# Performance work log

Measured on AMD Instinct MI355X. Metric: run time of the kernel, lower is better.

Reference implementation:

```python
import jax, jax.numpy as jnp
import numpy as np

H, QK, V, HID = 24, 16, 16, 128
EPS = 1e-6


def setup_inputs() -> dict:
    key = jax.random.key(0)
    ks = jax.random.split(key, 12)
    N, L = 2, 512
    s = 0.05
    inp = {
        "x": jax.random.normal(ks[0], (N, L, HID), jnp.float32),
        "R": jax.random.normal(ks[1], (N, L, 3, 3), jnp.float32),
        "t": jax.random.normal(ks[2], (N, L, 3), jnp.float32) * 10.0,
        "mask": jnp.ones((N, L), bool),
        # torch nn.Linear weights are (out_features, in_features)
        "Wq": jax.random.normal(ks[3], (H * QK, HID), jnp.float32) * s,
        "Wk": jax.random.normal(ks[4], (H * QK, HID), jnp.float32) * s,
        "Wv": jax.random.normal(ks[5], (H * V, HID), jnp.float32) * s,
        "bv": jnp.zeros((H * V,), jnp.float32),
        "Wa": jax.random.normal(ks[6], (3 * H, HID), jnp.float32) * s,
        "ba": jnp.full((3 * H,), EPS, jnp.float32),
        "Wb": jax.random.normal(ks[7], (3 * H, HID), jnp.float32) * s,
        "bb": jnp.full((3 * H,), EPS, jnp.float32),
        "Wp": jax.random.normal(ks[8], (HID, (V + 5) * H), jnp.float32) * s,
        "bp": jnp.zeros((HID,), jnp.float32),
        "alpha": -2.0 * jnp.ones((1, H, 1, 1), jnp.float32),
        "beta": -2.0 * jnp.ones((1, H, 1, 1), jnp.float32),
    }
    return inp


def reference(x, R, t, mask, Wq, Wk, Wv, bv, Wa, ba, Wb, bb, Wp, bp, alpha, beta):
    N, L, _ = x.shape
    al = jax.nn.softplus(alpha)  # (1,H,1,1)
    be = jax.nn.softplus(beta)

    a = (x @ Wa.T + ba).reshape(N, L, H, 1, 3).transpose(0, 2, 1, 3, 4)  # (N,H,L,1,3)
    b = (x @ Wb.T + bb).reshape(N, L, H, 1, 3).transpose(0, 2, 1, 3, 4)  # (N,H,L,1,3)

    # to_local: express t_j in local frame of residue i -> R_i^T (t_j - t_i)
    rel = t[:, None, :, :] - t[:, :, None, :]              # (N,L,L,3)
    local = jnp.einsum('nidx,nijd->nijx', R, rel)          # (N,L,L,3)

    r = local[:, None] - b                                  # (N,H,L,L,3)
    r_size = jnp.sqrt(jnp.sum(r * r, axis=-1))              # (N,H,L,L)
    a_size = jnp.sqrt(jnp.sum(a * a, axis=-1))              # (N,H,L,1)
    r_dot_a = jnp.sum(r * a, axis=-1)                       # (N,H,L,L)
    theta = jnp.arccos(r_dot_a / ((r_size + EPS) * (a_size + EPS)))

    ray_w = -al * r_size - be * theta                       # (N,H,L,L)

    q = (x @ Wq.T).reshape(N, L, H, QK)
    k = (x @ Wk.T).reshape(N, L, H, QK)
    std_w = jnp.einsum('nihd,njhd->nhij', q, k) * (QK ** -0.5)

    att = (2.0 ** -0.5) * (ray_w + std_w)
    diag = jnp.eye(L, dtype=bool)
    att = jnp.where(diag[None, None], jnp.asarray(-100.0, att.dtype), att)
    att = jnp.where(mask[:, None, None, :], att, -jnp.inf)
    att = jax.nn.softmax(att, axis=-1)                      # (N,H,L,L)

    v = (x @ Wv.T + bv).reshape(N, L, H, V)
    v_aggr = jnp.einsum('nhij,njhd->nihd', att, v)          # (N,L,H,V)
    r_aggr = jnp.einsum('nhij,nhijd->nihd', att, r)         # (N,L,H,3)
    r_aggr_size = jnp.sqrt(jnp.sum(r_aggr * r_aggr, axis=-1))  # (N,L,H)
    theta_aggr = jnp.einsum('nhij,nhij->nih', att, theta)   # (N,L,H)

    concat = jnp.concatenate([
        v_aggr.reshape(N, L, -1),
        r_aggr.reshape(N, L, -1),
        r_aggr_size,
        theta_aggr,
    ], axis=-1)                                             # (N,L,(V+5)*H)
    return concat @ Wp.T + bp
```

## Files before the change

kernel.cpp:

```cpp
#include <hip/hip_runtime.h>
#include <math.h>

#define NHEAD 24
#define LEN   512
#define NB    2
#define HID   128
#define EPSI  1e-6f

static constexpr size_t QKV_SZ = (size_t)NB * NHEAD * LEN * 16;
static constexpr size_t AB_SZ  = (size_t)NB * NHEAD * LEN * 3;
static constexpr size_t Q_OFF = 0;
static constexpr size_t K_OFF = QKV_SZ;
static constexpr size_t V_OFF = 2 * QKV_SZ;
static constexpr size_t A_OFF = 3 * QKV_SZ;
static constexpr size_t B_OFF = A_OFF + AB_SZ;
static constexpr size_t C_OFF = B_OFF + AB_SZ;

#define QSCALE2 0.25504597f
#define SCL     1.02020406f
#define CSHIFT  (-14.4269504f)

__device__ __forceinline__ float fast_exp2(float x) {
    return __builtin_amdgcn_exp2f(x);
}

__global__ __launch_bounds__(256) void proj_kernel(
    const float* __restrict__ x,
    const float* __restrict__ Wq, const float* __restrict__ Wk,
    const float* __restrict__ Wv, const float* __restrict__ bv,
    const float* __restrict__ Wa, const float* __restrict__ ba,
    const float* __restrict__ Wb, const float* __restrict__ bb,
    float* __restrict__ ws)
{
    __shared__ float xs[16][132];
    const int tid  = threadIdx.x;
    const int pos0 = blockIdx.y * 16;

    {
        const float* src = x + (size_t)pos0 * HID;
        int f = tid * 4;
        float4 v0 = *(const float4*)(src + f);
        *(float4*)&xs[f >> 7][f & 127] = v0;
        f += 1024;
        float4 v1 = *(const float4*)(src + f);
        *(float4*)&xs[f >> 7][f & 127] = v1;
    }
    __syncthreads();

    const int r_loc = tid >> 4;
    const int p_loc = tid & 15;
    const int row   = blockIdx.x * 16 + r_loc;
    const int pos   = pos0 + p_loc;
    const int n = pos >> 9;
    const int j = pos & (LEN - 1);

    const float* wrow;
    float bias = 0.f, scale = 1.f;
    float* outp;
    if (row < 384) {
        const int h = row >> 4, d = row & 15;
        wrow = Wq + (size_t)row * HID; scale = QSCALE2;
        outp = (float*)ws + Q_OFF + ((((size_t)(n*NHEAD + h))*LEN + j) << 4) + d;
    } else if (row < 768) {
        const int r = row - 384, h = r >> 4, d = r & 15;
        wrow = Wk + (size_t)r * HID;
        outp = (float*)ws + K_OFF + ((((size_t)(n*NHEAD + h))*LEN + j) << 4) + d;
    } else if (row < 1152) {
        const int r = row - 768, h = r >> 4, d = r & 15;
        wrow = Wv + (size_t)r * HID; bias = bv[r];
        outp = (float*)ws + V_OFF + ((((size_t)(n*NHEAD + h))*LEN + j) << 4) + d;
    } else if (row < 1224) {
        const int r = row - 1152, h = r / 3, c = r - h*3;
        wrow = Wa + (size_t)r * HID; bias = ba[r];
        outp = (float*)ws + A_OFF + (((size_t)(n*NHEAD + h))*LEN + j)*3 + c;
    } else {
        const int r = row - 1224, h = r / 3, c = r - h*3;
        wrow = Wb + (size_t)r * HID; bias = bb[r];
        outp = (float*)ws + B_OFF + (((size_t)(n*NHEAD + h))*LEN + j)*3 + c;
    }

    float acc = 0.f;
    #pragma unroll
    for (int c = 0; c < HID; c += 4) {
        float4 w  = *(const float4*)(wrow + c);
        float4 xv = *(const float4*)&xs[p_loc][c];
        acc += w.x * xv.x + w.y * xv.y + w.z * xv.z + w.w * xv.w;
    }
    *outp = acc * scale + bias;
}

__global__ __launch_bounds__(256) void attn_kernel(
    const float* __restrict__ Rm, const float* __restrict__ tg,
    const float* __restrict__ alpha, const float* __restrict__ beta,
    const float* __restrict__ ws, float* __restrict__ conc)
{
    __shared__ float ks[2][64*20];
    __shared__ float vs[2][64*20];
    __shared__ float tsh[512*4];

    const int tid   = threadIdx.x;
    const int lane  = tid & 63;
    const int li    = lane & 15;
    const int g     = lane >> 4;
    const int bx    = blockIdx.x;
    const int nh    = bx >> 5;
    const int ibase = (bx & 31) << 4;
    const int h     = nh % NHEAD;
    const int n     = nh / NHEAD;
    const int i     = ibase + ((tid >> 6) << 2) + g;
    const int iloc  = i & 63;
    const int dtile = ibase >> 6;

    const size_t nh16 = (size_t)nh * LEN * 16;
    const float* kg   = ws + K_OFF + nh16;
    const float* vg   = ws + V_OFF + nh16;
    const float* tng  = tg + (size_t)n * LEN * 3;

    auto stage = [&](int tt, int b) {
        const int row = tid >> 2, c4 = (tid & 3) << 2;
        *(float4*)&ks[b][row*20 + c4] = *(const float4*)(kg + (size_t)tt*1024 + tid*4);
        *(float4*)&vs[b][row*20 + c4] = *(const float4*)(vg + (size_t)tt*1024 + tid*4);
    };

    for (int idx = tid; idx < LEN; idx += 256) {
        const float t0 = tng[idx*3+0], t1 = tng[idx*3+1], t2 = tng[idx*3+2];
        *(float4*)&tsh[idx<<2] = make_float4(t0, t1, t2, 0.f);
    }
    stage(0, 0);

    const size_t ni = (size_t)n * LEN + i;
    const float* Ri = Rm + ni * 9;
    const float R00 = Ri[0], R01 = Ri[1], R02 = Ri[2];
    const float R10 = Ri[3], R11 = Ri[4], R12 = Ri[5];
    const float R20 = Ri[6], R21 = Ri[7], R22 = Ri[8];
    const float ti0 = tng[i*3+0], ti1 = tng[i*3+1], ti2 = tng[i*3+2];

    const float* bpn = ws + B_OFF + ((size_t)nh*LEN + i)*3;
    const float c0 = -(R00*ti0 + R10*ti1 + R20*ti2) - bpn[0];
    const float c1 = -(R01*ti0 + R11*ti1 + R21*ti2) - bpn[1];
    const float c2 = -(R02*ti0 + R12*ti1 + R22*ti2) - bpn[2];

    const float* ap = ws + A_OFF + ((size_t)nh*LEN + i)*3;
    const float a0 = ap[0], a1 = ap[1], a2 = ap[2];
    const float inv_as = 1.0f / (sqrtf(a0*a0 + a1*a1 + a2*a2) + EPSI);
    const float an0 = a0*inv_as, an1 = a1*inv_as, an2 = a2*inv_as;

    const float4* qp = (const float4*)(ws + Q_OFF + nh16 + ((size_t)i << 4));
    const float4 q0 = qp[0], q1 = qp[1], q2 = qp[2], q3 = qp[3];

    const float al2n = -SCL * log1pf(__expf(alpha[h]));
    const float be2n = -SCL * log1pf(__expf(beta[h]));

    float ssum = 0.f, thacc = 0.f;
    float racc0 = 0.f, racc1 = 0.f, racc2 = 0.f;
    float vacc[16];
    #pragma unroll
    for (int d = 0; d < 16; ++d) vacc[d] = 0.f;

    __syncthreads();

    for (int tt = 0; tt < 8; ++tt) {
        const int cur = tt & 1;
        if (tt < 7) stage(tt + 1, cur ^ 1);
        const bool isdiag = (tt == dtile);

        #pragma unroll
        for (int sub = 0; sub < 4; ++sub) {
            const int jl = li + (sub << 4);
            const float4 tj = *(const float4*)&tsh[((tt << 6) + jl) << 2];

            const float r0 = fmaf(R00,tj.x, fmaf(R10,tj.y, fmaf(R20,tj.z, c0)));
            const float r1 = fmaf(R01,tj.x, fmaf(R11,tj.y, fmaf(R21,tj.z, c1)));
            const float r2 = fmaf(R02,tj.x, fmaf(R12,tj.y, fmaf(R22,tj.z, c2)));
            const float rs  = sqrtf(fmaf(r0,r0, fmaf(r1,r1, r2*r2)));
            const float rda = fmaf(r0,an0, fmaf(r1,an1, r2*an2));
            float carg = rda * __builtin_amdgcn_rcpf(rs + EPSI);
            carg = fminf(1.f, fmaxf(-1.f, carg));
            const float u = fabsf(carg);
            const float thp = sqrtf(1.f - u) *
                (1.5707288f + u*(-0.2121144f + u*(0.0742610f - 0.0187293f*u)));
            const float theta = (carg >= 0.f) ? thp : (3.14159265f - thp);

            const float* kb = &ks[cur][jl*20];
            const float4 k0 = *(const float4*)(kb+0),  k1 = *(const float4*)(kb+4);
            const float4 k2 = *(const float4*)(kb+8),  k3 = *(const float4*)(kb+12);
            float qk = q0.x*k0.x;
            qk = fmaf(q0.y,k0.y, qk); qk = fmaf(q0.z,k0.z, qk); qk = fmaf(q0.w,k0.w, qk);
            qk = fmaf(q1.x,k1.x, qk); qk = fmaf(q1.y,k1.y, qk); qk = fmaf(q1.z,k1.z, qk); qk = fmaf(q1.w,k1.w, qk);
            qk = fmaf(q2.x,k2.x, qk); qk = fmaf(q2.y,k2.y, qk); qk = fmaf(q2.z,k2.z, qk); qk = fmaf(q2.w,k2.w, qk);
            qk = fmaf(q3.x,k3.x, qk); qk = fmaf(q3.y,k3.y, qk); qk = fmaf(q3.z,k3.z, qk); qk = fmaf(q3.w,k3.w, qk);

            float sc = fmaf(be2n, theta, fmaf(al2n, rs, qk)) + CSHIFT;
            float p  = fast_exp2(sc);
            if (isdiag && jl == iloc) p = 0.f;

            const float* vb = &vs[cur][jl*20];
            const float4 v0 = *(const float4*)(vb+0),  v1 = *(const float4*)(vb+4);
            const float4 v2 = *(const float4*)(vb+8),  v3 = *(const float4*)(vb+12);

            ssum += p;
            vacc[0]  = fmaf(p,v0.x,vacc[0]);  vacc[1]  = fmaf(p,v0.y,vacc[1]);
            vacc[2]  = fmaf(p,v0.z,vacc[2]);  vacc[3]  = fmaf(p,v0.w,vacc[3]);
            vacc[4]  = fmaf(p,v1.x,vacc[4]);  vacc[5]  = fmaf(p,v1.y,vacc[5]);
            vacc[6]  = fmaf(p,v1.z,vacc[6]);  vacc[7]  = fmaf(p,v1.w,vacc[7]);
            vacc[8]  = fmaf(p,v2.x,vacc[8]);  vacc[9]  = fmaf(p,v2.y,vacc[9]);
            vacc[10] = fmaf(p,v2.z,vacc[10]); vacc[11] = fmaf(p,v2.w,vacc[11]);
            vacc[12] = fmaf(p,v3.x,vacc[12]); vacc[13] = fmaf(p,v3.y,vacc[13]);
            vacc[14] = fmaf(p,v3.z,vacc[14]); vacc[15] = fmaf(p,v3.w,vacc[15]);
            racc0 = fmaf(p,r0,racc0); racc1 = fmaf(p,r1,racc1); racc2 = fmaf(p,r2,racc2);
            thacc = fmaf(p,theta,thacc);
        }
        __syncthreads();
    }

    #pragma unroll
    for (int msk = 1; msk < 16; msk <<= 1) {
        ssum  += __shfl_xor(ssum,  msk, 16);
        #pragma unroll
        for (int d = 0; d < 16; ++d) vacc[d] += __shfl_xor(vacc[d], msk, 16);
        racc0 += __shfl_xor(racc0, msk, 16);
        racc1 += __shfl_xor(racc1, msk, 16);
        racc2 += __shfl_xor(racc2, msk, 16);
        thacc += __shfl_xor(thacc, msk, 16);
    }

    if (li == 0) {
        const float inv = 1.0f / ssum;
        float* cb = conc + ni * 504;
        #pragma unroll
        for (int d = 0; d < 16; ++d) cb[(h<<4) + d] = vacc[d] * inv;
        const float ra0 = racc0*inv, ra1 = racc1*inv, ra2 = racc2*inv;
        cb[384 + h*3 + 0] = ra0;
        cb[384 + h*3 + 1] = ra1;
        cb[384 + h*3 + 2] = ra2;
        cb[456 + h] = sqrtf(ra0*ra0 + ra1*ra1 + ra2*ra2);
        cb[480 + h] = thacc * inv;
    }
}

__global__ __launch_bounds__(256) void outproj_kernel(
    const float* __restrict__ conc, const float* __restrict__ Wp,
    const float* __restrict__ bp, float* __restrict__ out)
{
    __shared__ float Csh[64][60];
    __shared__ float Wsh[32][60];
    const int tid    = threadIdx.x;
    const int p_base = blockIdx.x * 64;
    const int o_base = blockIdx.y * 32;
    const int kc     = blockIdx.z * 56;
    const int p0 = tid >> 4, ob = tid & 15;

    for (int f = tid; f < 64*14; f += 256) {
        const int row = f / 14, c4 = (f - row*14) << 2;
        *(float4*)&Csh[row][c4] =
            *(const float4*)(conc + (size_t)(p_base + row)*504 + kc + c4);
    }
    for (int f = tid; f < 32*14; f += 256) {
        const int row = f / 14, c4 = (f - row*14) << 2;
        *(float4*)&Wsh[row][c4] =
            *(const float4*)(Wp + (size_t)(o_base + row)*504 + kc + c4);
    }
    __syncthreads();

    float acc[4][2];
    #pragma unroll
    for (int m = 0; m < 4; ++m) { acc[m][0] = 0.f; acc[m][1] = 0.f; }

    #pragma unroll
    for (int k4 = 0; k4 < 14; ++k4) {
        float4 xv[4], wv[2];
        #pragma unroll
        for (int m = 0; m < 4; ++m) xv[m] = *(float4*)&Csh[p0 + 16*m][k4*4];
        #pragma unroll
        for (int o = 0; o < 2; ++o) wv[o] = *(float4*)&Wsh[ob + 16*o][k4*4];
        #pragma unroll
        for (int m = 0; m < 4; ++m)
            #pragma unroll
            for (int o = 0; o < 2; ++o)
                acc[m][o] += xv[m].x*wv[o].x + xv[m].y*wv[o].y +
                             xv[m].z*wv[o].z + xv[m].w*wv[o].w;
    }

    const bool first = (blockIdx.z == 0);
    #pragma unroll
    for (int m = 0; m < 4; ++m) {
        const int p = p_base + p0 + 16*m;
        #pragma unroll
        for (int o = 0; o < 2; ++o) {
            const int oo = o_base + ob + 16*o;
            const float add = acc[m][o] + (first ? bp[oo] : 0.f);
            atomicAdd(&out[(size_t)p*HID + oo], add);
        }
    }
}

extern "C" void kernel_launch(void* const* d_in, const int* in_sizes, int n_in,
                              void* d_out, int out_size, void* d_ws, size_t ws_size,
                              hipStream_t stream) {
    const float* x     = (const float*)d_in[0];
    const float* R     = (const float*)d_in[1];
    const float* t     = (const float*)d_in[2];
    const float* Wq    = (const float*)d_in[4];
    const float* Wk    = (const float*)d_in[5];
    const float* Wv    = (const float*)d_in[6];
    const float* bv    = (const float*)d_in[7];
    const float* Wa    = (const float*)d_in[8];
    const float* ba    = (const float*)d_in[9];
    const float* Wb    = (const float*)d_in[10];
    const float* bb    = (const float*)d_in[11];
    const float* Wp    = (const float*)d_in[12];
    const float* bp    = (const float*)d_in[13];
    const float* alpha = (const float*)d_in[14];
    const float* beta  = (const float*)d_in[15];

    float* ws  = (float*)d_ws;
    float* out = (float*)d_out;

    hipMemsetAsync(out, 0, (size_t)out_size * sizeof(float), stream);

    proj_kernel<<<dim3(81, 64), 256, 0, stream>>>(
        x, Wq, Wk, Wv, bv, Wa, ba, Wb, bb, ws);

    attn_kernel<<<(NB * NHEAD * LEN) / 16, 256, 0, stream>>>(
        R, t, alpha, beta, ws, ws + C_OFF);

    outproj_kernel<<<dim3(16, 4, 9), 256, 0, stream>>>(ws + C_OFF, Wp, bp, out);
}
```

Before: 173.7 us.

## Register-tile projection GEMM with shared W/X tiles and stream t per tile

The projection kernel now loads a 32-row weight tile and a 64-position input tile into shared memory, and each thread computes a 2x4 register block instead of a single dot product read straight from global weights. This cuts global weight traffic and raises arithmetic intensity, using fewer, larger blocks. The attention kernel stops preloading all 512 translation vectors into LDS. It instead stages a 64-entry t tile alongside the K/V double buffer, which reduces LDS use and removes the prologue loop. The tradeoff is more LDS per projection block and fewer blocks to spread across CUs.

```diff
diff --git a/kernel.cpp b/kernel.cpp
--- a/kernel.cpp
+++ b/kernel.cpp
@@ -24,6 +24,30 @@
     return __builtin_amdgcn_exp2f(x);
 }
 
+__device__ __forceinline__ void store_proj(int rg, int pos, float val,
+    const float* __restrict__ bv, const float* __restrict__ ba,
+    const float* __restrict__ bb, float* __restrict__ ws)
+{
+    const int n = pos >> 9;
+    const int j = pos & (LEN - 1);
+    if (rg < 384) {
+        const int h = rg >> 4, d = rg & 15;
+        ws[Q_OFF + ((((size_t)(n*NHEAD + h))*LEN + j) << 4) + d] = val * QSCALE2;
+    } else if (rg < 768) {
+        const int r = rg - 384, h = r >> 4, d = r & 15;
+        ws[K_OFF + ((((size_t)(n*NHEAD + h))*LEN + j) << 4) + d] = val;
+    } else if (rg < 1152) {
+        const int r = rg - 768, h = r >> 4, d = r & 15;
+        ws[V_OFF + ((((size_t)(n*NHEAD + h))*LEN + j) << 4) + d] = val + bv[r];
+    } else if (rg < 1224) {
+        const int r = rg - 1152, h = r / 3, c = r - h*3;
+        ws[A_OFF + (((size_t)(n*NHEAD + h))*LEN + j)*3 + c] = val + ba[r];
+    } else {
+        const int r = rg - 1224, h = r / 3, c = r - h*3;
+        ws[B_OFF + (((size_t)(n*NHEAD + h))*LEN + j)*3 + c] = val + bb[r];
+    }
+}
+
 __global__ __launch_bounds__(256) void proj_kernel(
     const float* __restrict__ x,
     const float* __restrict__ Wq, const float* __restrict__ Wk,
@@ -32,61 +56,67 @@
     const float* __restrict__ Wb, const float* __restrict__ bb,
     float* __restrict__ ws)
 {
-    __shared__ float xs[16][132];
-    const int tid  = threadIdx.x;
-    const int pos0 = blockIdx.y * 16;
-
-    {
-        const float* src = x + (size_t)pos0 * HID;
-        int f = tid * 4;
-        float4 v0 = *(const float4*)(src + f);
-        *(float4*)&xs[f >> 7][f & 127] = v0;
-        f += 1024;
-        float4 v1 = *(const float4*)(src + f);
-        *(float4*)&xs[f >> 7][f & 127] = v1;
+    __shared__ float Wsh[32][132];
+    __shared__ float Xsh[64][132];
+    const int tid    = threadIdx.x;
+    const int r_base = blockIdx.x * 32;
+    const int p_base = blockIdx.y * 64;
+
+    #pragma unroll
+    for (int it = 0; it < 4; ++it) {
+        const int f = tid + 256*it;
+        const int row = f >> 5, c4 = (f & 31) << 2;
+        int rg = r_base + row;
+        if (rg >= 1296) rg = 0;
+        const float* src;
+        if      (rg < 384)  src = Wq + (size_t)rg*HID;
+        else if (rg < 768)  src = Wk + (size_t)(rg-384)*HID;
+        else if (rg < 1152) src = Wv + (size_t)(rg-768)*HID;
+        else if (rg < 1224) src = Wa + (size_t)(rg-1152)*HID;
+        else                src = Wb + (size_t)(rg-1224)*HID;
+        *(float4*)&Wsh[row][c4] = *(const float4*)(src + c4);
+    }
+    #pragma unroll
+    for (int it = 0; it < 8; ++it) {
+        const int f = tid + 256*it;
+        const int row = f >> 5, c4 = (f & 31) << 2;
+        *(float4*)&Xsh[row][c4] =
+            *(const float4*)(x + (size_t)(p_base + row)*HID + c4);
     }
     __syncthreads();
 
-    const int r_loc = tid >> 4;
-    const int p_loc = tid & 15;
-    const int row   = blockIdx.x * 16 + r_loc;
-    const int pos   = pos0 + p_loc;
-    const int n = pos >> 9;
-    const int j = pos & (LEN - 1);
-
-    const float* wrow;
-    float bias = 0.f, scale = 1.f;
-    float* outp;
-    if (row < 384) {
-        const int h = row >> 4, d = row & 15;
-        wrow = Wq + (size_t)row * HID; scale = QSCALE2;
-        outp = (float*)ws + Q_OFF + ((((size_t)(n*NHEAD + h))*LEN + j) << 4) + d;
-    } else if (row < 768) {
-        const int r = row - 384, h = r >> 4, d = r & 15;
-        wrow = Wk + (size_t)r * HID;
-        outp = (float*)ws + K_OFF + ((((size_t)(n*NHEAD + h))*LEN + j) << 4) + d;
-    } else if (row < 1152) {
-        const int r = row - 768, h = r >> 4, d = r & 15;
-        wrow = Wv + (size_t)r * HID; bias = bv[r];
-        outp = (float*)ws + V_OFF + ((((size_t)(n*NHEAD + h))*LEN + j) << 4) + d;
-    } else if (row < 1224) {
-        const int r = row - 1152, h = r / 3, c = r - h*3;
-        wrow = Wa + (size_t)r * HID; bias = ba[r];
-        outp = (float*)ws + A_OFF + (((size_t)(n*NHEAD + h))*LEN + j)*3 + c;
-    } else {
-        const int r = row - 1224, h = r / 3, c = r - h*3;
-        wrow = Wb + (size_t)r * HID; bias = bb[r];
-        outp = (float*)ws + B_OFF + (((size_t)(n*NHEAD + h))*LEN + j)*3 + c;
-    }
-
-    float acc = 0.f;
-    #pragma unroll
-    for (int c = 0; c < HID; c += 4) {
-        float4 w  = *(const float4*)(wrow + c);
-        float4 xv = *(const float4*)&xs[p_loc][c];
-        acc += w.x * xv.x + w.y * xv.y + w.z * xv.z + w.w * xv.w;
-    }
-    *outp = acc * scale + bias;
+    const int a0 = tid >> 4;
+    const int p0 = tid & 15;
+
+    float acc[2][4];
+    #pragma unroll
+    for (int m = 0; m < 2; ++m)
+        #pragma unroll
+        for (int q = 0; q < 4; ++q) acc[m][q] = 0.f;
+
+    #pragma unroll
+    for (int k4 = 0; k4 < 32; ++k4) {
+        float4 wv[2], xv[4];
+        #pragma unroll
+        for (int m = 0; m < 2; ++m) wv[m] = *(float4*)&Wsh[a0 + 16*m][k4*4];
+        #pragma unroll
+        for (int q = 0; q < 4; ++q) xv[q] = *(float4*)&Xsh[p0 + 16*q][k4*4];
+        #pragma unroll
+        for (int m = 0; m < 2; ++m)
+            #pragma unroll
+            for (int q = 0; q < 4; ++q)
+                acc[m][q] = fmaf(wv[m].x, xv[q].x, fmaf(wv[m].y, xv[q].y,
+                            fmaf(wv[m].z, xv[q].z, fmaf(wv[m].w, xv[q].w, acc[m][q]))));
+    }
+
+    #pragma unroll
+    for (int m = 0; m < 2; ++m) {
+        const int rg = r_base + a0 + 16*m;
+        if (rg >= 1296) continue;
+        #pragma unroll
+        for (int q = 0; q < 4; ++q)
+            store_proj(rg, p_base + p0 + 16*q, acc[m][q], bv, ba, bb, ws);
+    }
 }
 
 __global__ __launch_bounds__(256) void attn_kernel(
@@ -94,9 +124,9 @@
     const float* __restrict__ alpha, const float* __restrict__ beta,
     const float* __restrict__ ws, float* __restrict__ conc)
 {
-    __shared__ float ks[2][64*20];
-    __shared__ float vs[2][64*20];
-    __shared__ float tsh[512*4];
+    __shared__ float  ks[2][64*20];
+    __shared__ float  vs[2][64*20];
+    __shared__ float4 ts4[2][64];
 
     const int tid   = threadIdx.x;
     const int lane  = tid & 63;
@@ -120,12 +150,12 @@
         const int row = tid >> 2, c4 = (tid & 3) << 2;
         *(float4*)&ks[b][row*20 + c4] = *(const float4*)(kg + (size_t)tt*1024 + tid*4);
         *(float4*)&vs[b][row*20 + c4] = *(const float4*)(vg + (size_t)tt*1024 + tid*4);
+        if (tid < 64) {
+            const int j = (tt << 6) + tid;
+            ts4[b][tid] = make_float4(tng[j*3+0], tng[j*3+1], tng[j*3+2], 0.f);
+        }
     };
 
-    for (int idx = tid; idx < LEN; idx += 256) {
-        const float t0 = tng[idx*3+0], t1 = tng[idx*3+1], t2 = tng[idx*3+2];
-        *(float4*)&tsh[idx<<2] = make_float4(t0, t1, t2, 0.f);
-    }
     stage(0, 0);
 
     const size_t ni = (size_t)n * LEN + i;
@@ -167,7 +197,7 @@
         #pragma unroll
         for (int sub = 0; sub < 4; ++sub) {
             const int jl = li + (sub << 4);
-            const float4 tj = *(const float4*)&tsh[((tt << 6) + jl) << 2];
+            const float4 tj = ts4[cur][jl];
 
             const float r0 = fmaf(R00,tj.x, fmaf(R10,tj.y, fmaf(R20,tj.z, c0)));
             const float r1 = fmaf(R01,tj.x, fmaf(R11,tj.y, fmaf(R21,tj.z, c1)));
@@ -318,7 +348,7 @@
 
     hipMemsetAsync(out, 0, (size_t)out_size * sizeof(float), stream);
 
-    proj_kernel<<<dim3(81, 64), 256, 0, stream>>>(
+    proj_kernel<<<dim3(41, 16), 256, 0, stream>>>(
         x, Wq, Wk, Wv, bv, Wa, ba, Wb, bb, ws);
 
     attn_kernel<<<(NB * NHEAD * LEN) / 16, 256, 0, stream>>>(
```

Result: slower. 307.8 us (+77.2%).

## Fuse projection, attention and output projection into one cooperative persistent kernel

Applied to the files above, without the earlier changes.

Merges the three kernels and the memset into one persistent kernel launched cooperatively, using grid-wide syncs between the projection, attention and output-projection phases, with shared memory unioned across phases. Attention now stages the t coordinates per tile alongside K/V instead of loading all 512 up front, which shrinks shared memory to allow more resident blocks. It is meant to remove launch overhead and inter-kernel gaps, but adds grid-sync cost, may lower occupancy through the larger merged register footprint, and limits the grid to resident blocks. A three-launch fallback remains if the cooperative launch fails.

```diff
diff --git a/kernel.cpp b/kernel.cpp
--- a/kernel.cpp
+++ b/kernel.cpp
@@ -1,5 +1,8 @@
 #include <hip/hip_runtime.h>
+#include <hip/hip_cooperative_groups.h>
 #include <math.h>
+
+namespace cg = cooperative_groups;
 
 #define NHEAD 24
 #define LEN   512
@@ -24,272 +27,284 @@
     return __builtin_amdgcn_exp2f(x);
 }
 
-__global__ __launch_bounds__(256) void proj_kernel(
-    const float* __restrict__ x,
+union SharedU {
+    struct { float Xsh[16][132]; } pj;
+    struct { float ks[2][1280]; float vs[2][1280]; float4 ts4[2][64]; } at;
+    struct { float Csh[64][60];  float Wsh[32][60]; } op;
+};
+
+__global__ __launch_bounds__(256, 6) void fused_all_kernel(
+    const float* __restrict__ x,  const float* __restrict__ Rm,
+    const float* __restrict__ tg,
     const float* __restrict__ Wq, const float* __restrict__ Wk,
     const float* __restrict__ Wv, const float* __restrict__ bv,
     const float* __restrict__ Wa, const float* __restrict__ ba,
     const float* __restrict__ Wb, const float* __restrict__ bb,
-    float* __restrict__ ws)
+    const float* __restrict__ Wp, const float* __restrict__ bp,
+    const float* __restrict__ alpha, const float* __restrict__ beta,
+    float* __restrict__ ws, float* __restrict__ out, int mode)
 {
-    __shared__ float xs[16][132];
+    __shared__ SharedU sh;
     const int tid  = threadIdx.x;
-    const int pos0 = blockIdx.y * 16;
-
-    {
-        const float* src = x + (size_t)pos0 * HID;
-        int f = tid * 4;
-        float4 v0 = *(const float4*)(src + f);
-        *(float4*)&xs[f >> 7][f & 127] = v0;
-        f += 1024;
-        float4 v1 = *(const float4*)(src + f);
-        *(float4*)&xs[f >> 7][f & 127] = v1;
-    }
-    __syncthreads();
-
-    const int r_loc = tid >> 4;
-    const int p_loc = tid & 15;
-    const int row   = blockIdx.x * 16 + r_loc;
-    const int pos   = pos0 + p_loc;
-    const int n = pos >> 9;
-    const int j = pos & (LEN - 1);
-
-    const float* wrow;
-    float bias = 0.f, scale = 1.f;
-    float* outp;
-    if (row < 384) {
-        const int h = row >> 4, d = row & 15;
-        wrow = Wq + (size_t)row * HID; scale = QSCALE2;
-        outp = (float*)ws + Q_OFF + ((((size_t)(n*NHEAD + h))*LEN + j) << 4) + d;
-    } else if (row < 768) {
-        const int r = row - 384, h = r >> 4, d = r & 15;
-        wrow = Wk + (size_t)r * HID;
-        outp = (float*)ws + K_OFF + ((((size_t)(n*NHEAD + h))*LEN + j) << 4) + d;
-    } else if (row < 1152) {
-        const int r = row - 768, h = r >> 4, d = r & 15;
-        wrow = Wv + (size_t)r * HID; bias = bv[r];
-        outp = (float*)ws + V_OFF + ((((size_t)(n*NHEAD + h))*LEN + j) << 4) + d;
-    } else if (row < 1224) {
-        const int r = row - 1152, h = r / 3, c = r - h*3;
-        wrow = Wa + (size_t)r * HID; bias = ba[r];
-        outp = (float*)ws + A_OFF + (((size_t)(n*NHEAD + h))*LEN + j)*3 + c;
-    } else {
-        const int r = row - 1224, h = r / 3, c = r - h*3;
-        wrow = Wb + (size_t)r * HID; bias = bb[r];
-        outp = (float*)ws + B_OFF + (((size_t)(n*NHEAD + h))*LEN + j)*3 + c;
-    }
-
-    float acc = 0.f;
-    #pragma unroll
-    for (int c = 0; c < HID; c += 4) {
-        float4 w  = *(const float4*)(wrow + c);
-        float4 xv = *(const float4*)&xs[p_loc][c];
-        acc += w.x * xv.x + w.y * xv.y + w.z * xv.z + w.w * xv.w;
-    }
-    *outp = acc * scale + bias;
-}
-
-__global__ __launch_bounds__(256) void attn_kernel(
-    const float* __restrict__ Rm, const float* __restrict__ tg,
-    const float* __restrict__ alpha, const float* __restrict__ beta,
-    const float* __restrict__ ws, float* __restrict__ conc)
-{
-    __shared__ float ks[2][64*20];
-    __shared__ float vs[2][64*20];
-    __shared__ float tsh[512*4];
-
-    const int tid   = threadIdx.x;
-    const int lane  = tid & 63;
-    const int li    = lane & 15;
-    const int g     = lane >> 4;
-    const int bx    = blockIdx.x;
-    const int nh    = bx >> 5;
-    const int ibase = (bx & 31) << 4;
-    const int h     = nh % NHEAD;
-    const int n     = nh / NHEAD;
-    const int i     = ibase + ((tid >> 6) << 2) + g;
-    const int iloc  = i & 63;
-    const int dtile = ibase >> 6;
-
-    const size_t nh16 = (size_t)nh * LEN * 16;
-    const float* kg   = ws + K_OFF + nh16;
-    const float* vg   = ws + V_OFF + nh16;
-    const float* tng  = tg + (size_t)n * LEN * 3;
-
-    auto stage = [&](int tt, int b) {
-        const int row = tid >> 2, c4 = (tid & 3) << 2;
-        *(float4*)&ks[b][row*20 + c4] = *(const float4*)(kg + (size_t)tt*1024 + tid*4);
-        *(float4*)&vs[b][row*20 + c4] = *(const float4*)(vg + (size_t)tt*1024 + tid*4);
-    };
-
-    for (int idx = tid; idx < LEN; idx += 256) {
-        const float t0 = tng[idx*3+0], t1 = tng[idx*3+1], t2 = tng[idx*3+2];
-        *(float4*)&tsh[idx<<2] = make_float4(t0, t1, t2, 0.f);
-    }
-    stage(0, 0);
-
-    const size_t ni = (size_t)n * LEN + i;
-    const float* Ri = Rm + ni * 9;
-    const float R00 = Ri[0], R01 = Ri[1], R02 = Ri[2];
-    const float R10 = Ri[3], R11 = Ri[4], R12 = Ri[5];
-    const float R20 = Ri[6], R21 = Ri[7], R22 = Ri[8];
-    const float ti0 = tng[i*3+0], ti1 = tng[i*3+1], ti2 = tng[i*3+2];
-
-    const float* bpn = ws + B_OFF + ((size_t)nh*LEN + i)*3;
-    const float c0 = -(R00*ti0 + R10*ti1 + R20*ti2) - bpn[0];
-    const float c1 = -(R01*ti0 + R11*ti1 + R21*ti2) - bpn[1];
-    const float c2 = -(R02*ti0 + R12*ti1 + R22*ti2) - bpn[2];
-
-    const float* ap = ws + A_OFF + ((size_t)nh*LEN + i)*3;
-    const float a0 = ap[0], a1 = ap[1], a2 = ap[2];
-    const float inv_as = 1.0f / (sqrtf(a0*a0 + a1*a1 + a2*a2) + EPSI);
-    const float an0 = a0*inv_as, an1 = a1*inv_as, an2 = a2*inv_as;
-
-    const float4* qp = (const float4*)(ws + Q_OFF + nh16 + ((size_t)i << 4));
-    const float4 q0 = qp[0], q1 = qp[1], q2 = qp[2], q3 = qp[3];
-
-    const float al2n = -SCL * log1pf(__expf(alpha[h]));
-    const float be2n = -SCL * log1pf(__expf(beta[h]));
-
-    float ssum = 0.f, thacc = 0.f;
-    float racc0 = 0.f, racc1 = 0.f, racc2 = 0.f;
-    float vacc[16];
-    #pragma unroll
-    for (int d = 0; d < 16; ++d) vacc[d] = 0.f;
-
-    __syncthreads();
-
-    for (int tt = 0; tt < 8; ++tt) {
-        const int cur = tt & 1;
-        if (tt < 7) stage(tt + 1, cur ^ 1);
-        const bool isdiag = (tt == dtile);
-
-        #pragma unroll
-        for (int sub = 0; sub < 4; ++sub) {
-            const int jl = li + (sub << 4);
-            const float4 tj = *(const float4*)&tsh[((tt << 6) + jl) << 2];
-
-            const float r0 = fmaf(R00,tj.x, fmaf(R10,tj.y, fmaf(R20,tj.z, c0)));
-            const float r1 = fmaf(R01,tj.x, fmaf(R11,tj.y, fmaf(R21,tj.z, c1)));
-            const float r2 = fmaf(R02,tj.x, fmaf(R12,tj.y, fmaf(R22,tj.z, c2)));
-            const float rs  = sqrtf(fmaf(r0,r0, fmaf(r1,r1, r2*r2)));
-            const float rda = fmaf(r0,an0, fmaf(r1,an1, r2*an2));
-            float carg = rda * __builtin_amdgcn_rcpf(rs + EPSI);
-            carg = fminf(1.f, fmaxf(-1.f, carg));
-            const float u = fabsf(carg);
-            const float thp = sqrtf(1.f - u) *
-                (1.5707288f + u*(-0.2121144f + u*(0.0742610f - 0.0187293f*u)));
-            const float theta = (carg >= 0.f) ? thp : (3.14159265f - thp);
-
-            const float* kb = &ks[cur][jl*20];
-            const float4 k0 = *(const float4*)(kb+0),  k1 = *(const float4*)(kb+4);
-            const float4 k2 = *(const float4*)(kb+8),  k3 = *(const float4*)(kb+12);
-            float qk = q0.x*k0.x;
-            qk = fmaf(q0.y,k0.y, qk); qk = fmaf(q0.z,k0.z, qk); qk = fmaf(q0.w,k0.w, qk);
-            qk = fmaf(q1.x,k1.x, qk); qk = fmaf(q1.y,k1.y, qk); qk = fmaf(q1.z,k1.z, qk); qk = fmaf(q1.w,k1.w, qk);
-            qk = fmaf(q2.x,k2.x, qk); qk = fmaf(q2.y,k2.y, qk); qk = fmaf(q2.z,k2.z, qk); qk = fmaf(q2.w,k2.w, qk);
-            qk = fmaf(q3.x,k3.x, qk); qk = fmaf(q3.y,k3.y, qk); qk = fmaf(q3.z,k3.z, qk); qk = fmaf(q3.w,k3.w, qk);
-
-            float sc = fmaf(be2n, theta, fmaf(al2n, rs, qk)) + CSHIFT;
-            float p  = fast_exp2(sc);
-            if (isdiag && jl == iloc) p = 0.f;
-
-            const float* vb = &vs[cur][jl*20];
-            const float4 v0 = *(const float4*)(vb+0),  v1 = *(const float4*)(vb+4);
-            const float4 v2 = *(const float4*)(vb+8),  v3 = *(const float4*)(vb+12);
-
-            ssum += p;
-            vacc[0]  = fmaf(p,v0.x,vacc[0]);  vacc[1]  = fmaf(p,v0.y,vacc[1]);
-            vacc[2]  = fmaf(p,v0.z,vacc[2]);  vacc[3]  = fmaf(p,v0.w,vacc[3]);
-            vacc[4]  = fmaf(p,v1.x,vacc[4]);  vacc[5]  = fmaf(p,v1.y,vacc[5]);
-            vacc[6]  = fmaf(p,v1.z,vacc[6]);  vacc[7]  = fmaf(p,v1.w,vacc[7]);
-            vacc[8]  = fmaf(p,v2.x,vacc[8]);  vacc[9]  = fmaf(p,v2.y,vacc[9]);
-            vacc[10] = fmaf(p,v2.z,vacc[10]); vacc[11] = fmaf(p,v2.w,vacc[11]);
-            vacc[12] = fmaf(p,v3.x,vacc[12]); vacc[13] = fmaf(p,v3.y,vacc[13]);
-            vacc[14] = fmaf(p,v3.z,vacc[14]); vacc[15] = fmaf(p,v3.w,vacc[15]);
-            racc0 = fmaf(p,r0,racc0); racc1 = fmaf(p,r1,racc1); racc2 = fmaf(p,r2,racc2);
-            thacc = fmaf(p,theta,thacc);
+    const int gdim = gridDim.x;
+
+    if (mode <= 1) {
+        for (int g = blockIdx.x * 256 + tid; g < NB * LEN * HID; g += gdim * 256)
+            out[g] = 0.f;
+
+        for (int tile = blockIdx.x; tile < 81 * 64; tile += gdim) {
+            const int rb   = (tile >> 6) << 4;
+            const int pos0 = (tile & 63) << 4;
+
+            #pragma unroll
+            for (int it = 0; it < 2; ++it) {
+                const int f = tid + 256 * it;
+                const int row = f >> 5, c4 = (f & 31) << 2;
+                *(float4*)&sh.pj.Xsh[row][c4] =
+                    *(const float4*)(x + (size_t)(pos0 + row) * HID + c4);
+            }
+            __syncthreads();
+
+            const int r_loc = tid >> 4, p_loc = tid & 15;
+            const int rg  = rb + r_loc;
+            const int pos = pos0 + p_loc;
+            const int n = pos >> 9, j = pos & (LEN - 1);
+
+            const float* wrow;
+            float bias = 0.f, scale = 1.f;
+            float* dst;
+            if (rg < 384) {
+                const int h = rg >> 4, d = rg & 15;
+                wrow = Wq + (size_t)rg * HID; scale = QSCALE2;
+                dst = ws + Q_OFF + ((((size_t)(n*NHEAD + h))*LEN + j) << 4) + d;
+            } else if (rg < 768) {
+                const int r = rg - 384, h = r >> 4, d = r & 15;
+                wrow = Wk + (size_t)r * HID;
+                dst = ws + K_OFF + ((((size_t)(n*NHEAD + h))*LEN + j) << 4) + d;
+            } else if (rg < 1152) {
+                const int r = rg - 768, h = r >> 4, d = r & 15;
+                wrow = Wv + (size_t)r * HID; bias = bv[r];
+                dst = ws + V_OFF + ((((size_t)(n*NHEAD + h))*LEN + j) << 4) + d;
+            } else if (rg < 1224) {
+                const int r = rg - 1152, h = r / 3, c = r - h*3;
+                wrow = Wa + (size_t)r * HID; bias = ba[r];
+                dst = ws + A_OFF + (((size_t)(n*NHEAD + h))*LEN + j)*3 + c;
+            } else {
+                const int r = rg - 1224, h = r / 3, c = r - h*3;
+                wrow = Wb + (size_t)r * HID; bias = bb[r];
+                dst = ws + B_OFF + (((size_t)(n*NHEAD + h))*LEN + j)*3 + c;
+            }
+
+            float acc = 0.f;
+            #pragma unroll 8
+            for (int c = 0; c < HID; c += 4) {
+                const float4 w  = *(const float4*)(wrow + c);
+                const float4 xv = *(const float4*)&sh.pj.Xsh[p_loc][c];
+                acc = fmaf(w.x, xv.x, fmaf(w.y, xv.y,
+                      fmaf(w.z, xv.z, fmaf(w.w, xv.w, acc))));
+            }
+            *dst = acc * scale + bias;
+            __syncthreads();
         }
-        __syncthreads();
-    }
-
-    #pragma unroll
-    for (int msk = 1; msk < 16; msk <<= 1) {
-        ssum  += __shfl_xor(ssum,  msk, 16);
-        #pragma unroll
-        for (int d = 0; d < 16; ++d) vacc[d] += __shfl_xor(vacc[d], msk, 16);
-        racc0 += __shfl_xor(racc0, msk, 16);
-        racc1 += __shfl_xor(racc1, msk, 16);
-        racc2 += __shfl_xor(racc2, msk, 16);
-        thacc += __shfl_xor(thacc, msk, 16);
-    }
-
-    if (li == 0) {
-        const float inv = 1.0f / ssum;
-        float* cb = conc + ni * 504;
-        #pragma unroll
-        for (int d = 0; d < 16; ++d) cb[(h<<4) + d] = vacc[d] * inv;
-        const float ra0 = racc0*inv, ra1 = racc1*inv, ra2 = racc2*inv;
-        cb[384 + h*3 + 0] = ra0;
-        cb[384 + h*3 + 1] = ra1;
-        cb[384 + h*3 + 2] = ra2;
-        cb[456 + h] = sqrtf(ra0*ra0 + ra1*ra1 + ra2*ra2);
-        cb[480 + h] = thacc * inv;
-    }
-}
-
-__global__ __launch_bounds__(256) void outproj_kernel(
-    const float* __restrict__ conc, const float* __restrict__ Wp,
-    const float* __restrict__ bp, float* __restrict__ out)
-{
-    __shared__ float Csh[64][60];
-    __shared__ float Wsh[32][60];
-    const int tid    = threadIdx.x;
-    const int p_base = blockIdx.x * 64;
-    const int o_base = blockIdx.y * 32;
-    const int kc     = blockIdx.z * 56;
-    const int p0 = tid >> 4, ob = tid & 15;
-
-    for (int f = tid; f < 64*14; f += 256) {
-        const int row = f / 14, c4 = (f - row*14) << 2;
-        *(float4*)&Csh[row][c4] =
-            *(const float4*)(conc + (size_t)(p_base + row)*504 + kc + c4);
-    }
-    for (int f = tid; f < 32*14; f += 256) {
-        const int row = f / 14, c4 = (f - row*14) << 2;
-        *(float4*)&Wsh[row][c4] =
-            *(const float4*)(Wp + (size_t)(o_base + row)*504 + kc + c4);
-    }
-    __syncthreads();
-
-    float acc[4][2];
-    #pragma unroll
-    for (int m = 0; m < 4; ++m) { acc[m][0] = 0.f; acc[m][1] = 0.f; }
-
-    #pragma unroll
-    for (int k4 = 0; k4 < 14; ++k4) {
-        float4 xv[4], wv[2];
-        #pragma unroll
-        for (int m = 0; m < 4; ++m) xv[m] = *(float4*)&Csh[p0 + 16*m][k4*4];
-        #pragma unroll
-        for (int o = 0; o < 2; ++o) wv[o] = *(float4*)&Wsh[ob + 16*o][k4*4];
-        #pragma unroll
-        for (int m = 0; m < 4; ++m)
-            #pragma unroll
-            for (int o = 0; o < 2; ++o)
-                acc[m][o] += xv[m].x*wv[o].x + xv[m].y*wv[o].y +
-                             xv[m].z*wv[o].z + xv[m].w*wv[o].w;
-    }
-
-    const bool first = (blockIdx.z == 0);
-    #pragma unroll
-    for (int m = 0; m < 4; ++m) {
-        const int p = p_base + p0 + 16*m;
-        #pragma unroll
-        for (int o = 0; o < 2; ++o) {
-            const int oo = o_base + ob + 16*o;
-            const float add = acc[m][o] + (first ? bp[oo] : 0.f);
-            atomicAdd(&out[(size_t)p*HID + oo], add);
+    }
+
+    if (mode == 0) cg::this_grid().sync();
+
+    if (mode == 0 || mode == 2) {
+        for (int unit = blockIdx.x; unit < NB * NHEAD * 32; unit += gdim) {
+            const int lane  = tid & 63;
+            const int li    = lane & 15;
+            const int g     = lane >> 4;
+            const int nh    = unit >> 5;
+            const int ibase = (unit & 31) << 4;
+            const int h     = nh % NHEAD;
+            const int n     = nh / NHEAD;
+            const int i     = ibase + ((tid >> 6) << 2) + g;
+            const int iloc  = i & 63;
+            const int dtile = ibase >> 6;
+
+            const size_t nh16 = (size_t)nh * LEN * 16;
+            const float* kg   = ws + K_OFF + nh16;
+            const float* vg   = ws + V_OFF + nh16;
+            const float* tng  = tg + (size_t)n * LEN * 3;
+
+            auto stage = [&](int tt, int b) {
+                const int row = tid >> 2, c4 = (tid & 3) << 2;
+                *(float4*)&sh.at.ks[b][row*20 + c4] = *(const float4*)(kg + (size_t)tt*1024 + tid*4);
+                *(float4*)&sh.at.vs[b][row*20 + c4] = *(const float4*)(vg + (size_t)tt*1024 + tid*4);
+                if (tid < 64) {
+                    const int j = (tt << 6) + tid;
+                    sh.at.ts4[b][tid] = make_float4(tng[j*3+0], tng[j*3+1], tng[j*3+2], 0.f);
+                }
+            };
+
+            stage(0, 0);
+
+            const size_t ni = (size_t)n * LEN + i;
+            const float* Ri = Rm + ni * 9;
+            const float R00 = Ri[0], R01 = Ri[1], R02 = Ri[2];
+            const float R10 = Ri[3], R11 = Ri[4], R12 = Ri[5];
+            const float R20 = Ri[6], R21 = Ri[7], R22 = Ri[8];
+            const float ti0 = tng[i*3+0], ti1 = tng[i*3+1], ti2 = tng[i*3+2];
+
+            const float* bpn = ws + B_OFF + ((size_t)nh*LEN + i)*3;
+            const float c0 = -(R00*ti0 + R10*ti1 + R20*ti2) - bpn[0];
+            const float c1 = -(R01*ti0 + R11*ti1 + R21*ti2) - bpn[1];
+            const float c2 = -(R02*ti0 + R12*ti1 + R22*ti2) - bpn[2];
+
+            const float* ap = ws + A_OFF + ((size_t)nh*LEN + i)*3;
+            const float a0 = ap[0], a1 = ap[1], a2 = ap[2];
+            const float inv_as = 1.0f / (sqrtf(a0*a0 + a1*a1 + a2*a2) + EPSI);
+            const float an0 = a0*inv_as, an1 = a1*inv_as, an2 = a2*inv_as;
+
+            const float4* qp = (const float4*)(ws + Q_OFF + nh16 + ((size_t)i << 4));
+            const float4 q0 = qp[0], q1 = qp[1], q2 = qp[2], q3 = qp[3];
+
+            const float al2n = -SCL * log1pf(__expf(alpha[h]));
+            const float be2n = -SCL * log1pf(__expf(beta[h]));
+
+            float ssum = 0.f, thacc = 0.f;
+            float racc0 = 0.f, racc1 = 0.f, racc2 = 0.f;
+            float vacc[16];
+            #pragma unroll
+            for (int d = 0; d < 16; ++d) vacc[d] = 0.f;
+
+            __syncthreads();
+
+            for (int tt = 0; tt < 8; ++tt) {
+                const int cur = tt & 1;
+                if (tt < 7) stage(tt + 1, cur ^ 1);
+                const bool isdiag = (tt == dtile);
+
+                #pragma unroll
+                for (int sub = 0; sub < 4; ++sub) {
+                    const int jl = li + (sub << 4);
+                    const float4 tj = sh.at.ts4[cur][jl];
+
+                    const float r0 = fmaf(R00,tj.x, fmaf(R10,tj.y, fmaf(R20,tj.z, c0)));
+                    const float r1 = fmaf(R01,tj.x, fmaf(R11,tj.y, fmaf(R21,tj.z, c1)));
+                    const float r2 = fmaf(R02,tj.x, fmaf(R12,tj.y, fmaf(R22,tj.z, c2)));
+                    const float rs  = sqrtf(fmaf(r0,r0, fmaf(r1,r1, r2*r2)));
+                    const float rda = fmaf(r0,an0, fmaf(r1,an1, r2*an2));
+                    float carg = rda * __builtin_amdgcn_rcpf(rs + EPSI);
+                    carg = fminf(1.f, fmaxf(-1.f, carg));
+                    const float u = fabsf(carg);
+                    const float thp = sqrtf(1.f - u) *
+                        (1.5707288f + u*(-0.2121144f + u*(0.0742610f - 0.0187293f*u)));
+                    const float theta = (carg >= 0.f) ? thp : (3.14159265f - thp);
+
+                    const float* kb = &sh.at.ks[cur][jl*20];
+                    const float4 k0 = *(const float4*)(kb+0),  k1 = *(const float4*)(kb+4);
+                    const float4 k2 = *(const float4*)(kb+8),  k3 = *(const float4*)(kb+12);
+                    float qk = q0.x*k0.x;
+                    qk = fmaf(q0.y,k0.y, qk); qk = fmaf(q0.z,k0.z, qk); qk = fmaf(q0.w,k0.w, qk);
+                    qk = fmaf(q1.x,k1.x, qk); qk = fmaf(q1.y,k1.y, qk); qk = fmaf(q1.z,k1.z, qk); qk = fmaf(q1.w,k1.w, qk);
+                    qk = fmaf(q2.x,k2.x, qk); qk = fmaf(q2.y,k2.y, qk); qk = fmaf(q2.z,k2.z, qk); qk = fmaf(q2.w,k2.w, qk);
+                    qk = fmaf(q3.x,k3.x, qk); qk = fmaf(q3.y,k3.y, qk); qk = fmaf(q3.z,k3.z, qk); qk = fmaf(q3.w,k3.w, qk);
+
+                    float sc = fmaf(be2n, theta, fmaf(al2n, rs, qk)) + CSHIFT;
+                    float p  = fast_exp2(sc);
+                    if (isdiag && jl == iloc) p = 0.f;
+
+                    const float* vb = &sh.at.vs[cur][jl*20];
+                    const float4 v0 = *(const float4*)(vb+0),  v1 = *(const float4*)(vb+4);
+                    const float4 v2 = *(const float4*)(vb+8),  v3 = *(const float4*)(vb+12);
+
+                    ssum += p;
+                    vacc[0]  = fmaf(p,v0.x,vacc[0]);  vacc[1]  = fmaf(p,v0.y,vacc[1]);
+                    vacc[2]  = fmaf(p,v0.z,vacc[2]);  vacc[3]  = fmaf(p,v0.w,vacc[3]);
+                    vacc[4]  = fmaf(p,v1.x,vacc[4]);  vacc[5]  = fmaf(p,v1.y,vacc[5]);
+                    vacc[6]  = fmaf(p,v1.z,vacc[6]);  vacc[7]  = fmaf(p,v1.w,vacc[7]);
+                    vacc[8]  = fmaf(p,v2.x,vacc[8]);  vacc[9]  = fmaf(p,v2.y,vacc[9]);
+                    vacc[10] = fmaf(p,v2.z,vacc[10]); vacc[11] = fmaf(p,v2.w,vacc[11]);
+                    vacc[12] = fmaf(p,v3.x,vacc[12]); vacc[13] = fmaf(p,v3.y,vacc[13]);
+                    vacc[14] = fmaf(p,v3.z,vacc[14]); vacc[15] = fmaf(p,v3.w,vacc[15]);
+                    racc0 = fmaf(p,r0,racc0); racc1 = fmaf(p,r1,racc1); racc2 = fmaf(p,r2,racc2);
+                    thacc = fmaf(p,theta,thacc);
+                }
+                __syncthreads();
+            }
+
+            #pragma unroll
+            for (int msk = 1; msk < 16; msk <<= 1) {
+                ssum  += __shfl_xor(ssum,  msk, 16);
+                #pragma unroll
+                for (int d = 0; d < 16; ++d) vacc[d] += __shfl_xor(vacc[d], msk, 16);
+                racc0 += __shfl_xor(racc0, msk, 16);
+                racc1 += __shfl_xor(racc1, msk, 16);
+                racc2 += __shfl_xor(racc2, msk, 16);
+                thacc += __shfl_xor(thacc, msk, 16);
+            }
+
+            if (li == 0) {
+                const float inv = 1.0f / ssum;
+                float* cb = ws + C_OFF + ni * 504;
+                #pragma unroll
+                for (int d = 0; d < 16; ++d) cb[(h<<4) + d] = vacc[d] * inv;
+                const float ra0 = racc0*inv, ra1 = racc1*inv, ra2 = racc2*inv;
+                cb[384 + h*3 + 0] = ra0;
+                cb[384 + h*3 + 1] = ra1;
+                cb[384 + h*3 + 2] = ra2;
+                cb[456 + h] = sqrtf(ra0*ra0 + ra1*ra1 + ra2*ra2);
+                cb[480 + h] = thacc * inv;
+            }
+            __syncthreads();
+        }
+    }
+
+    if (mode == 0) cg::this_grid().sync();
+
+    if (mode == 0 || mode == 3) {
+        const float* conc = ws + C_OFF;
+        for (int t3 = blockIdx.x; t3 < 576; t3 += gdim) {
+            const int p_base = (t3 & 15) * 64;
+            const int o_base = ((t3 >> 4) & 3) * 32;
+            const int kc     = (t3 >> 6) * 56;
+            const int p0 = tid >> 4, ob = tid & 15;
+
+            for (int f = tid; f < 64*14; f += 256) {
+                const int row = f / 14, c4 = (f - row*14) << 2;
+                *(float4*)&sh.op.Csh[row][c4] =
+                    *(const float4*)(conc + (size_t)(p_base + row)*504 + kc + c4);
+            }
+            for (int f = tid; f < 32*14; f += 256) {
+                const int row = f / 14, c4 = (f - row*14) << 2;
+                *(float4*)&sh.op.Wsh[row][c4] =
+                    *(const float4*)(Wp + (size_t)(o_base + row)*504 + kc + c4);
+            }
+            __syncthreads();
+
+            float acc[4][2];
+            #pragma unroll
+            for (int m = 0; m < 4; ++m) { acc[m][0] = 0.f; acc[m][1] = 0.f; }
+
+            #pragma unroll 2
+            for (int k4 = 0; k4 < 14; ++k4) {
+                float4 xv[4], wv[2];
+                #pragma unroll
+                for (int m = 0; m < 4; ++m) xv[m] = *(float4*)&sh.op.Csh[p0 + 16*m][k4*4];
+                #pragma unroll
+                for (int o = 0; o < 2; ++o) wv[o] = *(float4*)&sh.op.Wsh[ob + 16*o][k4*4];
+                #pragma unroll
+                for (int m = 0; m < 4; ++m)
+                    #pragma unroll
+                    for (int o = 0; o < 2; ++o)
+                        acc[m][o] += xv[m].x*wv[o].x + xv[m].y*wv[o].y +
+                                     xv[m].z*wv[o].z + xv[m].w*wv[o].w;
+            }
+
+            const bool first = (kc == 0);
+            #pragma unroll
+            for (int m = 0; m < 4; ++m) {
+                const int p = p_base + p0 + 16*m;
+                #pragma unroll
+                for (int o = 0; o < 2; ++o) {
+                    const int oo = o_base + ob + 16*o;
+                    const float add = acc[m][o] + (first ? bp[oo] : 0.f);
+                    atomicAdd(&out[(size_t)p*HID + oo], add);
+                }
+            }
+            __syncthreads();
         }
     }
 }
@@ -316,13 +331,34 @@
     float* ws  = (float*)d_ws;
     float* out = (float*)d_out;
 
-    hipMemsetAsync(out, 0, (size_t)out_size * sizeof(float), stream);
-
-    proj_kernel<<<dim3(81, 64), 256, 0, stream>>>(
-        x, Wq, Wk, Wv, bv, Wa, ba, Wb, bb, ws);
-
-    attn_kernel<<<(NB * NHEAD * LEN) / 16, 256, 0, stream>>>(
-        R, t, alpha, beta, ws, ws + C_OFF);
-
-    outproj_kernel<<<dim3(16, 4, 9), 256, 0, stream>>>(ws + C_OFF, Wp, bp, out);
+    int mode = 0;
+    void* args[] = {
+        (void*)&x, (void*)&R, (void*)&t,
+        (void*)&Wq, (void*)&Wk, (void*)&Wv, (void*)&bv,
+        (void*)&Wa, (void*)&ba, (void*)&Wb, (void*)&bb,
+        (void*)&Wp, (void*)&bp, (void*)&alpha, (void*)&beta,
+        (void*)&ws, (void*)&out, (void*)&mode
+    };
+
+    int occ = 0;
+    hipError_t qerr = hipOccupancyMaxActiveBlocksPerMultiprocessor(
+        &occ, fused_all_kernel, 256, 0);
+
+    bool launched = false;
+    if (qerr == hipSuccess && occ > 0) {
+        int grid = occ * 256;
+        if (grid > 1536) grid = 1536;
+        hipError_t lerr = hipLaunchCooperativeKernel(
+            (const void*)fused_all_kernel, dim3(grid), dim3(256), args, 0, stream);
+        launched = (lerr == hipSuccess);
+    }
+
+    if (!launched) {
+        fused_all_kernel<<<1536, 256, 0, stream>>>(
+            x, R, t, Wq, Wk, Wv, bv, Wa, ba, Wb, bb, Wp, bp, alpha, beta, ws, out, 1);
+        fused_all_kernel<<<1536, 256, 0, stream>>>(
+            x, R, t, Wq, Wk, Wv, bv, Wa, ba, Wb, bb, Wp, bp, alpha, beta, ws, out, 2);
+        fused_all_kernel<<<576, 256, 0, stream>>>(
+            x, R, t, Wq, Wk, Wv, bv, Wa, ba, Wb, bb, Wp, bp, alpha, beta, ws, out, 3);
+    }
 }
```

Result: slower. 442.0 us (+154.5%).
